# Optimization experiments

Hardware: AMD Instinct MI355X
Metric: run time of the kernel (lower is better)

## Reference

```python
import jax, jax.numpy as jnp
import numpy as np

B, N, F = 4096, 128, 3
EPS = 1e-5


def _bn(x, g, b):
    # BatchNorm1d(element_num) on [B, N, C]: channels are dim 1 (the N elements);
    # training-mode stats over dims (0, 2), biased variance (torch default).
    m = x.mean(axis=(0, 2), keepdims=True)
    v = ((x - m) ** 2).mean(axis=(0, 2), keepdims=True)
    return (x - m) / jnp.sqrt(v + EPS) * g[None, :, None] + b[None, :, None]


def _rel(x, W, bvec, psi, phi, wr):
    # f'_i = wr/N * sum_{j != i} (psi*phi * <x_i, x_j>) * relu(unary(x_j))
    n = x.shape[1]
    U = jax.nn.relu(jnp.einsum('bnd,ed->bne', x, W) + bvec)       # [B,N,D]
    S = (psi * phi) * jnp.einsum('bnd,bmd->bnm', x, x)            # [B,N,N]
    S = S * (1.0 - jnp.eye(n, dtype=x.dtype))                     # exclude j == i
    return wr * jnp.einsum('bnm,bmd->bnd', S, U) / n


def setup_inputs() -> dict:
    key = jax.random.key(0)
    ks = iter(jax.random.split(key, 64))
    d1, d2 = 2 * F, 4 * F  # 6, 12

    def w(shape, s=0.1):
        return (jax.random.normal(next(ks), shape, dtype=jnp.float32) * s)

    def scalar():
        return jax.random.uniform(next(ks), (), dtype=jnp.float32)

    inp = {
        'x': jax.random.normal(next(ks), (B, N, F), dtype=jnp.float32),
        'fc1_w': w((d1, F)), 'fc1_b': w((d1,)),
        'bn1_g': jnp.ones((N,), jnp.float32), 'bn1_b': jnp.zeros((N,), jnp.float32),
        'fc2_w': w((d2, d1)), 'fc2_b': w((d2,)),
        'bn2_g': jnp.ones((N,), jnp.float32), 'bn2_b': jnp.zeros((N,), jnp.float32),
        'fc3_w': w((d2, d2)), 'fc3_b': w((d2,)),
        'u1_w': w((d2, d2)), 'u1_b': w((d2,)), 'ps1': scalar(), 'ph1': scalar(), 'wr1': scalar(),
        'u2_w': w((d2, d2)), 'u2_b': w((d2,)), 'ps2': scalar(), 'ph2': scalar(), 'wr2': scalar(),
        'u3_w': w((d2, d2)), 'u3_b': w((d2,)), 'ps3': scalar(), 'ph3': scalar(), 'wr3': scalar(),
        'u4_w': w((d2, d2)), 'u4_b': w((d2,)), 'ps4': scalar(), 'ph4': scalar(), 'wr4': scalar(),
        'fc4_w': w((d1, d2)), 'fc4_b': w((d1,)),
        'bn4_g': jnp.ones((N,), jnp.float32), 'bn4_b': jnp.zeros((N,), jnp.float32),
        'fc5_w': w((F, d1)), 'fc5_b': w((F,)),
        'fc6_w': w((1, F)), 'fc6_b': w((1,)),
        'fc7_w': w((F - 1, F)), 'fc7_b': w((F - 1,)),
        'fc8_w': w((1, F)), 'fc8_b': w((1,)),
    }
    return inp


def reference(x, fc1_w, fc1_b, bn1_g, bn1_b, fc2_w, fc2_b, bn2_g, bn2_b,
              fc3_w, fc3_b,
              u1_w, u1_b, ps1, ph1, wr1,
              u2_w, u2_b, ps2, ph2, wr2,
              u3_w, u3_b, ps3, ph3, wr3,
              u4_w, u4_b, ps4, ph4, wr4,
              fc4_w, fc4_b, bn4_g, bn4_b,
              fc5_w, fc5_b, fc6_w, fc6_b, fc7_w, fc7_b, fc8_w, fc8_b):
    h = jax.nn.relu(_bn(jnp.einsum('bnf,ef->bne', x, fc1_w) + fc1_b, bn1_g, bn1_b))
    h = jax.nn.relu(_bn(jnp.einsum('bnf,ef->bne', h, fc2_w) + fc2_b, bn2_g, bn2_b))
    h = jax.nn.sigmoid(jnp.einsum('bnf,ef->bne', h, fc3_w) + fc3_b)
    h = _rel(h, u1_w, u1_b, ps1, ph1, wr1)
    h = _rel(h, u2_w, u2_b, ps2, ph2, wr2)
    h = _rel(h, u3_w, u3_b, ps3, ph3, wr3)
    h = _rel(h, u4_w, u4_b, ps4, ph4, wr4)
    h = jax.nn.relu(_bn(jnp.einsum('bnf,ef->bne', h, fc4_w) + fc4_b, bn4_g, bn4_b))
    h = jax.nn.relu(jnp.einsum('bnf,ef->bne', h, fc5_w) + fc5_b)
    cls = jnp.einsum('bnf,ef->bne', h, fc6_w) + fc6_b          # [B,N,1]
    geo = jnp.einsum('bnf,ef->bne', h, fc7_w) + fc7_b          # [B,N,F-1]
    res = jnp.concatenate([cls, geo], axis=2)                   # [B,N,F]
    pres = res.max(axis=1)                                      # MaxPool1d over all N -> [B,F]
    pred = jax.nn.sigmoid(pres @ fc8_w.T + fc8_b)               # [B,1]
    return pred
```

## Files before the change

kernel.cpp:

```cpp
#include <hip/hip_runtime.h>
#include <hip/hip_fp16.h>

#define BB 4096
#define NN 128
#define EPS 1e-5f

#define S1 0
#define S2 2048
#define S4 4096
#define A4_OFF 6144

static __device__ __forceinline__ float sigmoidf_(float z){
  return 1.f/(1.f+__expf(-z));
}
static __device__ __forceinline__ float2 h2f2_(unsigned u){
  __half2 h = *reinterpret_cast<__half2*>(&u);
  return __half22float2(h);
}

static __device__ __forceinline__ float fdot2_(unsigned a, unsigned b, float c){
#if defined(__has_builtin)
#if __has_builtin(__builtin_amdgcn_fdot2)
  typedef _Float16 h2v __attribute__((ext_vector_type(2)));
  h2v av = *reinterpret_cast<h2v*>(&a);
  h2v bv = *reinterpret_cast<h2v*>(&b);
  return __builtin_amdgcn_fdot2(av, bv, c, false);
#else
  float2 af = h2f2_(a), bf = h2f2_(b);
  return fmaf(af.y, bf.y, fmaf(af.x, bf.x, c));
#endif
#else
  float2 af = h2f2_(a), bf = h2f2_(b);
  return fmaf(af.y, bf.y, fmaf(af.x, bf.x, c));
#endif
}

__global__ __launch_bounds__(256) void k1(const float* __restrict__ x, const float* __restrict__ w1,
                   const float* __restrict__ b1, float* __restrict__ st){
  __shared__ float bl[512];
  const int t = threadIdx.x;
  const int tid = blockIdx.x*256 + t;
  float W[18], Bv[6];
  #pragma unroll
  for (int i=0;i<18;i++) W[i]=w1[i];
  #pragma unroll
  for (int i=0;i<6;i++) Bv[i]=b1[i];
  float s=0.f, sq=0.f;
  #pragma unroll
  for (int kk=0;kk<2;kk++){
    const int r = tid + kk*262144;
    const float* xr = x + (size_t)r*3;
    float x0=xr[0], x1=xr[1], x2=xr[2];
    #pragma unroll
    for (int e=0;e<6;e++){
      float a = fmaf(x0,W[e*3+0], fmaf(x1,W[e*3+1], fmaf(x2,W[e*3+2], Bv[e])));
      s+=a; sq=fmaf(a,a,sq);
    }
  }
  bl[t]=s; bl[256+t]=sq;
  __syncthreads();
  const int shadow = (blockIdx.x & 7)*256;
  if (t<128) atomicAdd(&st[S1+shadow+t], bl[t]+bl[t+128]);
  else       atomicAdd(&st[S1+shadow+t], bl[t+128]+bl[t+256]);
}

__global__ __launch_bounds__(256) void k2(const float* __restrict__ x,
                   const float* __restrict__ w1, const float* __restrict__ b1,
                   const float* __restrict__ g1, const float* __restrict__ bb1,
                   const float* __restrict__ w2, const float* __restrict__ b2,
                   float* __restrict__ st){
  __shared__ float bl[512];
  const int t = threadIdx.x;
  const int tid = blockIdx.x*256 + t;
  const int n = t & 127;
  float ss=0.f, qs=0.f;
  #pragma unroll
  for (int c=0;c<8;c++){ ss+=st[S1+c*256+n]; qs+=st[S1+c*256+128+n]; }
  const float mean = ss*(1.f/(BB*6));
  const float var  = qs*(1.f/(BB*6)) - mean*mean;
  const float sc = g1[n]*rsqrtf(var+EPS), sh = bb1[n]-mean*sc;
  float W1[18], B1v[6], W2[72], B2v[12];
  #pragma unroll
  for (int i=0;i<18;i++) W1[i]=w1[i];
  #pragma unroll
  for (int i=0;i<6;i++) B1v[i]=b1[i];
  #pragma unroll
  for (int i=0;i<72;i++) W2[i]=w2[i];
  #pragma unroll
  for (int i=0;i<12;i++) B2v[i]=b2[i];
  float s=0.f, sq=0.f;
  #pragma unroll
  for (int kk=0;kk<2;kk++){
    const int r = tid + kk*262144;
    const float* xr = x + (size_t)r*3;
    float x0=xr[0], x1=xr[1], x2=xr[2];
    float h[6];
    #pragma unroll
    for (int e=0;e<6;e++){
      float a = fmaf(x0,W1[e*3+0], fmaf(x1,W1[e*3+1], fmaf(x2,W1[e*3+2], B1v[e])));
      h[e]=fmaxf(fmaf(a,sc,sh),0.f);
    }
    #pragma unroll
    for (int d=0;d<12;d++){
      float z=B2v[d];
      #pragma unroll
      for (int e=0;e<6;e++) z=fmaf(h[e],W2[d*6+e],z);
      s+=z; sq=fmaf(z,z,sq);
    }
  }
  bl[t]=s; bl[256+t]=sq;
  __syncthreads();
  const int shadow = (blockIdx.x & 7)*256;
  if (t<128) atomicAdd(&st[S2+shadow+t], bl[t]+bl[t+128]);
  else       atomicAdd(&st[S2+shadow+t], bl[t+128]+bl[t+256]);
}

__global__ __launch_bounds__(256) void k3(
  const float* __restrict__ x,
  const float* __restrict__ w1, const float* __restrict__ b1,
  const float* __restrict__ g1, const float* __restrict__ bb1,
  const float* __restrict__ w2, const float* __restrict__ b2,
  const float* __restrict__ g2, const float* __restrict__ bb2,
  const float* __restrict__ w3, const float* __restrict__ b3,
  const float* __restrict__ u1w, const float* __restrict__ u1b,
  const float* __restrict__ ps1, const float* __restrict__ ph1, const float* __restrict__ wr1,
  const float* __restrict__ u2w, const float* __restrict__ u2b,
  const float* __restrict__ ps2, const float* __restrict__ ph2, const float* __restrict__ wr2,
  const float* __restrict__ u3w, const float* __restrict__ u3b,
  const float* __restrict__ ps3, const float* __restrict__ ph3, const float* __restrict__ wr3,
  const float* __restrict__ u4w, const float* __restrict__ u4b,
  const float* __restrict__ ps4, const float* __restrict__ ph4, const float* __restrict__ wr4,
  const float* __restrict__ w4, const float* __restrict__ b4,
  __half* __restrict__ a4, float* __restrict__ st)
{
  __shared__ float lds[4][1536];
  const int wave = threadIdx.x >> 6;
  const int lane = threadIdx.x & 63;
  const int b = blockIdx.x*4 + wave;
  unsigned* Xp = (unsigned*)&lds[wave][0];
  unsigned* Up = (unsigned*)&lds[wave][768];
  const int r0 = lane*2, r1 = r0+1;

  float s1a=0,q1a=0,s1b=0,q1b=0,s2a=0,q2a=0,s2b=0,q2b=0;
  #pragma unroll
  for (int c=0;c<8;c++){
    s1a+=st[S1+c*256+r0]; q1a+=st[S1+c*256+128+r0];
    s1b+=st[S1+c*256+r1]; q1b+=st[S1+c*256+128+r1];
    s2a+=st[S2+c*256+r0]; q2a+=st[S2+c*256+128+r0];
    s2b+=st[S2+c*256+r1]; q2b+=st[S2+c*256+128+r1];
  }
  const float inv1 = 1.f/(BB*6), inv2 = 1.f/(BB*12);
  float m = s1a*inv1, v = q1a*inv1 - m*m;
  const float sA0 = g1[r0]*rsqrtf(v+EPS), hA0 = bb1[r0]-m*sA0;
  m = s1b*inv1; v = q1b*inv1 - m*m;
  const float sA1 = g1[r1]*rsqrtf(v+EPS), hA1 = bb1[r1]-m*sA1;
  m = s2a*inv2; v = q2a*inv2 - m*m;
  const float sB0 = g2[r0]*rsqrtf(v+EPS), hB0 = bb2[r0]-m*sB0;
  m = s2b*inv2; v = q2b*inv2 - m*m;
  const float sB1 = g2[r1]*rsqrtf(v+EPS), hB1 = bb2[r1]-m*sB1;

  const float2* xr = (const float2*)(x + ((size_t)b*128 + r0)*3);
  float2 c0=xr[0], c1=xr[1], c2=xr[2];
  const float xa0=c0.x, xa1=c0.y, xa2=c1.x;
  const float xb0=c1.y, xb1=c2.x, xb2=c2.y;

  float X0[12], X1[12];
  {
    float g6a[6], g6b[6];
    #pragma unroll
    for (int e=0;e<6;e++){
      float a0 = fmaf(xa0,w1[e*3+0], fmaf(xa1,w1[e*3+1], fmaf(xa2,w1[e*3+2], b1[e])));
      float a1v= fmaf(xb0,w1[e*3+0], fmaf(xb1,w1[e*3+1], fmaf(xb2,w1[e*3+2], b1[e])));
      g6a[e]=fmaxf(fmaf(a0,sA0,hA0),0.f);
      g6b[e]=fmaxf(fmaf(a1v,sA1,hA1),0.f);
    }
    float h0[12], h1[12];
    #pragma unroll
    for (int d=0;d<12;d++){
      float z0=b2[d], z1=b2[d];
      #pragma unroll
      for (int e=0;e<6;e++){ z0=fmaf(g6a[e],w2[d*6+e],z0); z1=fmaf(g6b[e],w2[d*6+e],z1); }
      h0[d]=fmaxf(fmaf(z0,sB0,hB0),0.f);
      h1[d]=fmaxf(fmaf(z1,sB1,hB1),0.f);
    }
    #pragma unroll
    for (int d=0; d<12; d++){
      float z0=b3[d], z1=b3[d];
      #pragma unroll
      for (int e=0;e<12;e++){ z0=fmaf(h0[e],w3[d*12+e],z0); z1=fmaf(h1[e],w3[d*12+e],z1); }
      X0[d]=sigmoidf_(z0); X1[d]=sigmoidf_(z1);
    }
  }

  const float* UW[4]  = {u1w,u2w,u3w,u4w};
  const float* UBv[4] = {u1b,u2b,u3b,u4b};
  const float cf[4] = {
    wr1[0]*ps1[0]*ph1[0]*(1.f/128.f),
    wr2[0]*ps2[0]*ph2[0]*(1.f/128.f),
    wr3[0]*ps3[0]*ph3[0]*(1.f/128.f),
    wr4[0]*ps4[0]*ph4[0]*(1.f/128.f)
  };

  const int g = lane>>4;
  int kc = lane & 15; if (kc>11) kc=11;

  #pragma unroll
  for (int l=0;l<4;l++){
    const float* uw = UW[l];
    const float* ub = UBv[l];
    const float coef = cf[l];
    float Y0[12], Y1[12];
    {
      float U0[12], U1[12];
      #pragma unroll
      for (int d=0;d<12;d++){
        float z0=ub[d], z1=ub[d];
        #pragma unroll
        for (int e=0;e<12;e++){ z0=fmaf(X0[e],uw[d*12+e],z0); z1=fmaf(X1[e],uw[d*12+e],z1); }
        U0[d]=fmaxf(z0,0.f); U1[d]=fmaxf(z1,0.f);
      }
      float q0=0.f, q1=0.f;
      #pragma unroll
      for (int e=0;e<12;e++){ q0=fmaf(X0[e],X0[e],q0); q1=fmaf(X1[e],X1[e],q1); }
      __half2 hp[12], up[12];
      #pragma unroll
      for (int e=0;e<12;e++){
        hp[e] = __floats2half2_rn(X0[e],X1[e]);
        up[e] = __floats2half2_rn(U0[e],U1[e]);
      }
      {
        const uint4* hpv = (const uint4*)hp;
        const uint4* upv = (const uint4*)up;
        uint4* xw = (uint4*)(Xp + lane*12);
        uint4* uwp = (uint4*)(Up + lane*12);
        xw[0]=hpv[0]; xw[1]=hpv[1]; xw[2]=hpv[2];
        uwp[0]=upv[0]; uwp[1]=upv[1]; uwp[2]=upv[2];
      }
      const float q0c = coef*q0, q1c = coef*q1;
      #pragma unroll
      for (int d=0;d<12;d++){ Y0[d] = -q0c*U0[d]; Y1[d] = -q1c*U1[d]; }
    }

    float mp[12];
    #pragma unroll
    for (int d=0;d<12;d++) mp[d]=0.f;
    #pragma unroll
    for (int i=0;i<16;i++){
      const int p = (g<<4) | ((i+g)&15);
      const unsigned xv2 = Xp[p*12 + kc];
      const uint4* urow = (const uint4*)(Up + p*12);
      uint4 ua=urow[0], ub4=urow[1], uc=urow[2];
      mp[0]=fdot2_(xv2, ua.x, mp[0]);  mp[1]=fdot2_(xv2, ua.y, mp[1]);
      mp[2]=fdot2_(xv2, ua.z, mp[2]);  mp[3]=fdot2_(xv2, ua.w, mp[3]);
      mp[4]=fdot2_(xv2, ub4.x, mp[4]); mp[5]=fdot2_(xv2, ub4.y, mp[5]);
      mp[6]=fdot2_(xv2, ub4.z, mp[6]); mp[7]=fdot2_(xv2, ub4.w, mp[7]);
      mp[8]=fdot2_(xv2, uc.x, mp[8]);  mp[9]=fdot2_(xv2, uc.y, mp[9]);
      mp[10]=fdot2_(xv2, uc.z, mp[10]); mp[11]=fdot2_(xv2, uc.w, mp[11]);
    }
    #pragma unroll
    for (int d=0;d<12;d++) mp[d] += __shfl_xor(mp[d], 16, 64);
    #pragma unroll
    for (int d=0;d<12;d++) mp[d] += __shfl_xor(mp[d], 32, 64);
    #pragma unroll
    for (int d=0;d<12;d++) mp[d] *= coef;

    #pragma unroll
    for (int k=0;k<12;k++){
      const float xa = X0[k], xb = X1[k];
      #pragma unroll
      for (int d=0;d<12;d++){
        const float mv = __int_as_float(__builtin_amdgcn_readlane(__float_as_int(mp[d]), k));
        Y0[d]=fmaf(xa,mv,Y0[d]); Y1[d]=fmaf(xb,mv,Y1[d]);
      }
    }
    #pragma unroll
    for (int d=0;d<12;d++){ X0[d]=Y0[d]; X1[d]=Y1[d]; }
  }

  float z0[6], z1[6];
  float s0=0.f,sq0=0.f,s1=0.f,sq1=0.f;
  #pragma unroll
  for (int e=0;e<6;e++){
    float a0=b4[e], a1v=b4[e];
    #pragma unroll
    for (int d=0;d<12;d++){ a0=fmaf(X0[d],w4[e*12+d],a0); a1v=fmaf(X1[d],w4[e*12+d],a1v); }
    z0[e]=a0; z1[e]=a1v;
    s0+=a0; sq0=fmaf(a0,a0,sq0); s1+=a1v; sq1=fmaf(a1v,a1v,sq1);
  }
  {
    __half2 ha[6];
    ha[0]=__floats2half2_rn(z0[0],z0[1]); ha[1]=__floats2half2_rn(z0[2],z0[3]); ha[2]=__floats2half2_rn(z0[4],z0[5]);
    ha[3]=__floats2half2_rn(z1[0],z1[1]); ha[4]=__floats2half2_rn(z1[2],z1[3]); ha[5]=__floats2half2_rn(z1[4],z1[5]);
    const uint2* hv = (const uint2*)ha;
    uint2* aw = (uint2*)(a4 + ((size_t)b*128 + r0)*6);
    aw[0]=hv[0]; aw[1]=hv[1]; aw[2]=hv[2];
  }

  __syncthreads();
  lds[wave][r0]=s0; lds[wave][r1]=s1;
  lds[wave][128+r0]=sq0; lds[wave][128+r1]=sq1;
  __syncthreads();
  const int t = threadIdx.x;
  const int c = (blockIdx.x & 7)*256;
  atomicAdd(&st[S4 + c + t], lds[0][t]+lds[1][t]+lds[2][t]+lds[3][t]);
}

__global__ __launch_bounds__(256) void k4(
  const __half* __restrict__ a4, const float* __restrict__ g4, const float* __restrict__ bb4,
  const float* __restrict__ w5, const float* __restrict__ b5,
  const float* __restrict__ w6, const float* __restrict__ b6,
  const float* __restrict__ w7, const float* __restrict__ b7,
  const float* __restrict__ w8, const float* __restrict__ b8,
  const float* __restrict__ st, float* __restrict__ out)
{
  const int wave = threadIdx.x>>6, lane = threadIdx.x&63;
  const int b = blockIdx.x*4 + wave;
  const int r0 = lane*2, r1 = r0+1;
  float ss0=0.f, qq0=0.f, ss1=0.f, qq1=0.f;
  #pragma unroll
  for (int cc=0;cc<8;cc++){
    ss0 += st[S4+cc*256+r0];     qq0 += st[S4+cc*256+128+r0];
    ss1 += st[S4+cc*256+r1];     qq1 += st[S4+cc*256+128+r1];
  }
  const float inv = 1.f/(BB*6);
  const float mean0 = ss0*inv, var0 = qq0*inv - mean0*mean0;
  const float sc0 = g4[r0]*rsqrtf(var0+EPS), sh0 = bb4[r0]-mean0*sc0;
  const float mean1 = ss1*inv, var1 = qq1*inv - mean1*mean1;
  const float sc1 = g4[r1]*rsqrtf(var1+EPS), sh1 = bb4[r1]-mean1*sc1;

  const uint2* ar = (const uint2*)(a4 + ((size_t)b*128 + r0)*6);
  uint2 v0=ar[0], v1=ar[1], v2=ar[2];
  float2 f0=h2f2_(v0.x), f1=h2f2_(v0.y), f2=h2f2_(v1.x);
  float2 f3=h2f2_(v1.y), f4=h2f2_(v2.x), f5=h2f2_(v2.y);
  float h0[6] = {f0.x,f0.y,f1.x,f1.y,f2.x,f2.y};
  float h1[6] = {f3.x,f3.y,f4.x,f4.y,f5.x,f5.y};
  #pragma unroll
  for (int e=0;e<6;e++){
    h0[e]=fmaxf(fmaf(h0[e],sc0,sh0),0.f);
    h1[e]=fmaxf(fmaf(h1[e],sc1,sh1),0.f);
  }
  float mx[3];
  {
    float h5a[3], h5b[3];
    #pragma unroll
    for (int f=0;f<3;f++){
      float za=b5[f], zb=b5[f];
      #pragma unroll
      for (int e=0;e<6;e++){ za=fmaf(h0[e],w5[f*6+e],za); zb=fmaf(h1[e],w5[f*6+e],zb); }
      h5a[f]=fmaxf(za,0.f); h5b[f]=fmaxf(zb,0.f);
    }
    float ca=b6[0], cb=b6[0];
    float g0a=b7[0], g0b=b7[0], g1a=b7[1], g1b=b7[1];
    #pragma unroll
    for (int f=0;f<3;f++){
      ca=fmaf(h5a[f],w6[f],ca);   cb=fmaf(h5b[f],w6[f],cb);
      g0a=fmaf(h5a[f],w7[f],g0a); g0b=fmaf(h5b[f],w7[f],g0b);
      g1a=fmaf(h5a[f],w7[3+f],g1a); g1b=fmaf(h5b[f],w7[3+f],g1b);
    }
    mx[0]=fmaxf(ca,cb); mx[1]=fmaxf(g0a,g0b); mx[2]=fmaxf(g1a,g1b);
  }
  #pragma unroll
  for (int off=32; off>0; off>>=1){
    mx[0]=fmaxf(mx[0], __shfl_xor(mx[0],off,64));
    mx[1]=fmaxf(mx[1], __shfl_xor(mx[1],off,64));
    mx[2]=fmaxf(mx[2], __shfl_xor(mx[2],off,64));
  }
  if (lane==0){
    float z = b8[0] + mx[0]*w8[0] + mx[1]*w8[1] + mx[2]*w8[2];
    out[b]=sigmoidf_(z);
  }
}

extern "C" void kernel_launch(void* const* d_in, const int* in_sizes, int n_in,
                              void* d_out, int out_size, void* d_ws, size_t ws_size,
                              hipStream_t stream){
  const float* x   = (const float*)d_in[0];
  const float* f1w = (const float*)d_in[1];
  const float* f1b = (const float*)d_in[2];
  const float* g1  = (const float*)d_in[3];
  const float* bb1 = (const float*)d_in[4];
  const float* f2w = (const float*)d_in[5];
  const float* f2b = (const float*)d_in[6];
  const float* g2  = (const float*)d_in[7];
  const float* bb2 = (const float*)d_in[8];
  const float* f3w = (const float*)d_in[9];
  const float* f3b = (const float*)d_in[10];
  const float* u1w = (const float*)d_in[11];
  const float* u1b = (const float*)d_in[12];
  const float* ps1 = (const float*)d_in[13];
  const float* ph1 = (const float*)d_in[14];
  const float* wr1 = (const float*)d_in[15];
  const float* u2w = (const float*)d_in[16];
  const float* u2b = (const float*)d_in[17];
  const float* ps2 = (const float*)d_in[18];
  const float* ph2 = (const float*)d_in[19];
  const float* wr2 = (const float*)d_in[20];
  const float* u3w = (const float*)d_in[21];
  const float* u3b = (const float*)d_in[22];
  const float* ps3 = (const float*)d_in[23];
  const float* ph3 = (const float*)d_in[24];
  const float* wr3 = (const float*)d_in[25];
  const float* u4w = (const float*)d_in[26];
  const float* u4b = (const float*)d_in[27];
  const float* ps4 = (const float*)d_in[28];
  const float* ph4 = (const float*)d_in[29];
  const float* wr4 = (const float*)d_in[30];
  const float* f4w = (const float*)d_in[31];
  const float* f4b = (const float*)d_in[32];
  const float* g4  = (const float*)d_in[33];
  const float* bb4 = (const float*)d_in[34];
  const float* f5w = (const float*)d_in[35];
  const float* f5b = (const float*)d_in[36];
  const float* f6w = (const float*)d_in[37];
  const float* f6b = (const float*)d_in[38];
  const float* f7w = (const float*)d_in[39];
  const float* f7b = (const float*)d_in[40];
  const float* f8w = (const float*)d_in[41];
  const float* f8b = (const float*)d_in[42];

  float* wsf = (float*)d_ws;
  float* st  = wsf;
  __half* a4 = (__half*)(wsf + A4_OFF);
  float* out = (float*)d_out;

  k1<<<dim3(1024), dim3(256), 0, stream>>>(x, f1w, f1b, st);
  k2<<<dim3(1024), dim3(256), 0, stream>>>(x, f1w, f1b, g1, bb1, f2w, f2b, st);
  k3<<<dim3(1024), dim3(256), 0, stream>>>(x, f1w, f1b, g1, bb1, f2w, f2b, g2, bb2,
      f3w, f3b,
      u1w,u1b,ps1,ph1,wr1, u2w,u2b,ps2,ph2,wr2,
      u3w,u3b,ps3,ph3,wr3, u4w,u4b,ps4,ph4,wr4,
      f4w, f4b, a4, st);
  k4<<<dim3(1024), dim3(256), 0, stream>>>(a4, g4, bb4, f5w, f5b,
      f6w, f6b, f7w, f7b, f8w, f8b, st, out);
}
```

Baseline: 199.9 us.

## Fuse four kernels into one cooperative kernel with grid-wide syncs

Replaces the four-kernel pipeline with a single cooperative kernel. Each wave holds one batch's activations in registers across all phases, and grid.sync() separates the BatchNorm statistic reductions. This avoids recomputing the early layers in later kernels, the fp16 intermediate round-trip through global memory, and three kernel launches. The trade-off is grid-sync cost, plus a requirement that all 1024 blocks be co-resident (256 CUs x 4). If the cooperative launch fails, it falls back to the old kernels.

```diff
diff --git a/kernel.cpp b/kernel.cpp
--- a/kernel.cpp
+++ b/kernel.cpp
@@ -1,5 +1,8 @@
 #include <hip/hip_runtime.h>
 #include <hip/hip_fp16.h>
+#include <hip/hip_cooperative_groups.h>
+
+namespace cg = cooperative_groups;
 
 #define BB 4096
 #define NN 128
@@ -34,6 +37,286 @@
   return fmaf(af.y, bf.y, fmaf(af.x, bf.x, c));
 #endif
 }
+
+__global__ __launch_bounds__(256, 4) void kf(
+  const float* __restrict__ x,
+  const float* __restrict__ w1, const float* __restrict__ b1,
+  const float* __restrict__ g1, const float* __restrict__ bb1,
+  const float* __restrict__ w2, const float* __restrict__ b2,
+  const float* __restrict__ g2, const float* __restrict__ bb2,
+  const float* __restrict__ w3, const float* __restrict__ b3,
+  const float* __restrict__ u1w, const float* __restrict__ u1b,
+  const float* __restrict__ ps1, const float* __restrict__ ph1, const float* __restrict__ wr1,
+  const float* __restrict__ u2w, const float* __restrict__ u2b,
+  const float* __restrict__ ps2, const float* __restrict__ ph2, const float* __restrict__ wr2,
+  const float* __restrict__ u3w, const float* __restrict__ u3b,
+  const float* __restrict__ ps3, const float* __restrict__ ph3, const float* __restrict__ wr3,
+  const float* __restrict__ u4w, const float* __restrict__ u4b,
+  const float* __restrict__ ps4, const float* __restrict__ ph4, const float* __restrict__ wr4,
+  const float* __restrict__ w4, const float* __restrict__ b4,
+  const float* __restrict__ g4, const float* __restrict__ bb4,
+  const float* __restrict__ w5, const float* __restrict__ b5,
+  const float* __restrict__ w6, const float* __restrict__ b6,
+  const float* __restrict__ w7, const float* __restrict__ b7,
+  const float* __restrict__ w8, const float* __restrict__ b8,
+  float* __restrict__ st, float* __restrict__ out)
+{
+  cg::grid_group grid = cg::this_grid();
+  __shared__ float lds[4][1536];
+  const int t = threadIdx.x;
+  const int wave = t >> 6, lane = t & 63;
+  const int b = blockIdx.x*4 + wave;
+  const int r0 = lane*2, r1 = r0+1;
+  const int shadow = (blockIdx.x & 7)*256;
+  unsigned* Xp = (unsigned*)&lds[wave][0];
+  unsigned* Up = (unsigned*)&lds[wave][768];
+
+  const float2* xr = (const float2*)(x + ((size_t)b*128 + r0)*3);
+  float2 c0=xr[0], c1=xr[1], c2=xr[2];
+  const float xa0=c0.x, xa1=c0.y, xa2=c1.x;
+  const float xb0=c1.y, xb1=c2.x, xb2=c2.y;
+
+  float a6a[6], a6b[6];
+  {
+    float s0=0.f,q0=0.f,s1v=0.f,q1=0.f;
+    #pragma unroll
+    for (int e=0;e<6;e++){
+      float va = fmaf(xa0,w1[e*3+0], fmaf(xa1,w1[e*3+1], fmaf(xa2,w1[e*3+2], b1[e])));
+      float vb = fmaf(xb0,w1[e*3+0], fmaf(xb1,w1[e*3+1], fmaf(xb2,w1[e*3+2], b1[e])));
+      a6a[e]=va; a6b[e]=vb;
+      s0+=va; q0=fmaf(va,va,q0);
+      s1v+=vb; q1=fmaf(vb,vb,q1);
+    }
+    lds[wave][r0]=s0; lds[wave][r1]=s1v;
+    lds[wave][128+r0]=q0; lds[wave][128+r1]=q1;
+    __syncthreads();
+    atomicAdd(&st[S1 + shadow + t], lds[0][t]+lds[1][t]+lds[2][t]+lds[3][t]);
+  }
+  grid.sync();
+
+  float z0[12], z1[12];
+  {
+    float sa=0.f,qa=0.f,sb=0.f,qb=0.f;
+    #pragma unroll
+    for (int c=0;c<8;c++){
+      sa+=st[S1+c*256+r0]; qa+=st[S1+c*256+128+r0];
+      sb+=st[S1+c*256+r1]; qb+=st[S1+c*256+128+r1];
+    }
+    const float inv1 = 1.f/(BB*6);
+    float m=sa*inv1, v=qa*inv1-m*m;
+    const float sA0=g1[r0]*rsqrtf(v+EPS), hA0=bb1[r0]-m*sA0;
+    m=sb*inv1; v=qb*inv1-m*m;
+    const float sA1=g1[r1]*rsqrtf(v+EPS), hA1=bb1[r1]-m*sA1;
+
+    float h0[6], h1[6];
+    #pragma unroll
+    for (int e=0;e<6;e++){
+      h0[e]=fmaxf(fmaf(a6a[e],sA0,hA0),0.f);
+      h1[e]=fmaxf(fmaf(a6b[e],sA1,hA1),0.f);
+    }
+    float s0=0.f,q0=0.f,s1v=0.f,q1=0.f;
+    #pragma unroll
+    for (int d=0;d<12;d++){
+      float za=b2[d], zb=b2[d];
+      #pragma unroll
+      for (int e=0;e<6;e++){ za=fmaf(h0[e],w2[d*6+e],za); zb=fmaf(h1[e],w2[d*6+e],zb); }
+      z0[d]=za; z1[d]=zb;
+      s0+=za; q0=fmaf(za,za,q0);
+      s1v+=zb; q1=fmaf(zb,zb,q1);
+    }
+    lds[wave][r0]=s0; lds[wave][r1]=s1v;
+    lds[wave][128+r0]=q0; lds[wave][128+r1]=q1;
+    __syncthreads();
+    atomicAdd(&st[S2 + shadow + t], lds[0][t]+lds[1][t]+lds[2][t]+lds[3][t]);
+  }
+  grid.sync();
+
+  float X0[12], X1[12];
+  {
+    float sa=0.f,qa=0.f,sb=0.f,qb=0.f;
+    #pragma unroll
+    for (int c=0;c<8;c++){
+      sa+=st[S2+c*256+r0]; qa+=st[S2+c*256+128+r0];
+      sb+=st[S2+c*256+r1]; qb+=st[S2+c*256+128+r1];
+    }
+    const float inv2 = 1.f/(BB*12);
+    float m=sa*inv2, v=qa*inv2-m*m;
+    const float sB0=g2[r0]*rsqrtf(v+EPS), hB0=bb2[r0]-m*sB0;
+    m=sb*inv2; v=qb*inv2-m*m;
+    const float sB1=g2[r1]*rsqrtf(v+EPS), hB1=bb2[r1]-m*sB1;
+
+    float h0[12], h1[12];
+    #pragma unroll
+    for (int d=0;d<12;d++){
+      h0[d]=fmaxf(fmaf(z0[d],sB0,hB0),0.f);
+      h1[d]=fmaxf(fmaf(z1[d],sB1,hB1),0.f);
+    }
+    #pragma unroll
+    for (int d=0;d<12;d++){
+      float za=b3[d], zb=b3[d];
+      #pragma unroll
+      for (int e=0;e<12;e++){ za=fmaf(h0[e],w3[d*12+e],za); zb=fmaf(h1[e],w3[d*12+e],zb); }
+      X0[d]=sigmoidf_(za); X1[d]=sigmoidf_(zb);
+    }
+  }
+
+  const float* UW[4]  = {u1w,u2w,u3w,u4w};
+  const float* UBv[4] = {u1b,u2b,u3b,u4b};
+  const float cf[4] = {
+    wr1[0]*ps1[0]*ph1[0]*(1.f/128.f),
+    wr2[0]*ps2[0]*ph2[0]*(1.f/128.f),
+    wr3[0]*ps3[0]*ph3[0]*(1.f/128.f),
+    wr4[0]*ps4[0]*ph4[0]*(1.f/128.f)
+  };
+
+  const int g = lane>>4;
+  int kc = lane & 15; if (kc>11) kc=11;
+
+  #pragma unroll
+  for (int l=0;l<4;l++){
+    const float* uw = UW[l];
+    const float* ub = UBv[l];
+    const float coef = cf[l];
+    float Y0[12], Y1[12];
+    {
+      float U0[12], U1[12];
+      #pragma unroll
+      for (int d=0;d<12;d++){
+        float za=ub[d], zb=ub[d];
+        #pragma unroll
+        for (int e=0;e<12;e++){ za=fmaf(X0[e],uw[d*12+e],za); zb=fmaf(X1[e],uw[d*12+e],zb); }
+        U0[d]=fmaxf(za,0.f); U1[d]=fmaxf(zb,0.f);
+      }
+      float q0=0.f, q1=0.f;
+      #pragma unroll
+      for (int e=0;e<12;e++){ q0=fmaf(X0[e],X0[e],q0); q1=fmaf(X1[e],X1[e],q1); }
+      __half2 hp[12], up[12];
+      #pragma unroll
+      for (int e=0;e<12;e++){
+        hp[e] = __floats2half2_rn(X0[e],X1[e]);
+        up[e] = __floats2half2_rn(U0[e],U1[e]);
+      }
+      {
+        const uint4* hpv = (const uint4*)hp;
+        const uint4* upv = (const uint4*)up;
+        uint4* xw  = (uint4*)(Xp + lane*12);
+        uint4* uwp = (uint4*)(Up + lane*12);
+        xw[0]=hpv[0]; xw[1]=hpv[1]; xw[2]=hpv[2];
+        uwp[0]=upv[0]; uwp[1]=upv[1]; uwp[2]=upv[2];
+      }
+      const float q0c = coef*q0, q1c = coef*q1;
+      #pragma unroll
+      for (int d=0;d<12;d++){ Y0[d] = -q0c*U0[d]; Y1[d] = -q1c*U1[d]; }
+    }
+
+    float mp[12];
+    #pragma unroll
+    for (int d=0;d<12;d++) mp[d]=0.f;
+    #pragma unroll
+    for (int i=0;i<16;i++){
+      const int p = (g<<4) | ((i+g)&15);
+      const unsigned xv2 = Xp[p*12 + kc];
+      const uint4* urow = (const uint4*)(Up + p*12);
+      uint4 ua=urow[0], ub4=urow[1], uc=urow[2];
+      mp[0]=fdot2_(xv2, ua.x, mp[0]);  mp[1]=fdot2_(xv2, ua.y, mp[1]);
+      mp[2]=fdot2_(xv2, ua.z, mp[2]);  mp[3]=fdot2_(xv2, ua.w, mp[3]);
+      mp[4]=fdot2_(xv2, ub4.x, mp[4]); mp[5]=fdot2_(xv2, ub4.y, mp[5]);
+      mp[6]=fdot2_(xv2, ub4.z, mp[6]); mp[7]=fdot2_(xv2, ub4.w, mp[7]);
+      mp[8]=fdot2_(xv2, uc.x, mp[8]);  mp[9]=fdot2_(xv2, uc.y, mp[9]);
+      mp[10]=fdot2_(xv2, uc.z, mp[10]); mp[11]=fdot2_(xv2, uc.w, mp[11]);
+    }
+    #pragma unroll
+    for (int d=0;d<12;d++) mp[d] += __shfl_xor(mp[d], 16, 64);
+    #pragma unroll
+    for (int d=0;d<12;d++) mp[d] += __shfl_xor(mp[d], 32, 64);
+    #pragma unroll
+    for (int d=0;d<12;d++) mp[d] *= coef;
+
+    #pragma unroll
+    for (int k=0;k<12;k++){
+      const float xa = X0[k], xb = X1[k];
+      #pragma unroll
+      for (int d=0;d<12;d++){
+        const float mv = __int_as_float(__builtin_amdgcn_readlane(__float_as_int(mp[d]), k));
+        Y0[d]=fmaf(xa,mv,Y0[d]); Y1[d]=fmaf(xb,mv,Y1[d]);
+      }
+    }
+    #pragma unroll
+    for (int d=0;d<12;d++){ X0[d]=Y0[d]; X1[d]=Y1[d]; }
+  }
+
+  float z4a[6], z4b[6];
+  {
+    float s0=0.f,q0=0.f,s1v=0.f,q1=0.f;
+    #pragma unroll
+    for (int e=0;e<6;e++){
+      float a0=b4[e], a1v=b4[e];
+      #pragma unroll
+      for (int d=0;d<12;d++){ a0=fmaf(X0[d],w4[e*12+d],a0); a1v=fmaf(X1[d],w4[e*12+d],a1v); }
+      z4a[e]=a0; z4b[e]=a1v;
+      s0+=a0; q0=fmaf(a0,a0,q0);
+      s1v+=a1v; q1=fmaf(a1v,a1v,q1);
+    }
+    __syncthreads();
+    lds[wave][r0]=s0; lds[wave][r1]=s1v;
+    lds[wave][128+r0]=q0; lds[wave][128+r1]=q1;
+    __syncthreads();
+    atomicAdd(&st[S4 + shadow + t], lds[0][t]+lds[1][t]+lds[2][t]+lds[3][t]);
+  }
+  grid.sync();
+
+  {
+    float ss0=0.f,qq0=0.f,ss1=0.f,qq1=0.f;
+    #pragma unroll
+    for (int cc=0;cc<8;cc++){
+      ss0+=st[S4+cc*256+r0]; qq0+=st[S4+cc*256+128+r0];
+      ss1+=st[S4+cc*256+r1]; qq1+=st[S4+cc*256+128+r1];
+    }
+    const float inv = 1.f/(BB*6);
+    const float mean0=ss0*inv, var0=qq0*inv-mean0*mean0;
+    const float sc0=g4[r0]*rsqrtf(var0+EPS), sh0=bb4[r0]-mean0*sc0;
+    const float mean1=ss1*inv, var1=qq1*inv-mean1*mean1;
+    const float sc1=g4[r1]*rsqrtf(var1+EPS), sh1=bb4[r1]-mean1*sc1;
+
+    float h0[6], h1[6];
+    #pragma unroll
+    for (int e=0;e<6;e++){
+      h0[e]=fmaxf(fmaf(z4a[e],sc0,sh0),0.f);
+      h1[e]=fmaxf(fmaf(z4b[e],sc1,sh1),0.f);
+    }
+    float mx[3];
+    {
+      float h5a[3], h5b[3];
+      #pragma unroll
+      for (int f=0;f<3;f++){
+        float za=b5[f], zb=b5[f];
+        #pragma unroll
+        for (int e=0;e<6;e++){ za=fmaf(h0[e],w5[f*6+e],za); zb=fmaf(h1[e],w5[f*6+e],zb); }
+        h5a[f]=fmaxf(za,0.f); h5b[f]=fmaxf(zb,0.f);
+      }
+      float ca=b6[0], cb=b6[0];
+      float g0a=b7[0], g0b=b7[0], g1a=b7[1], g1b=b7[1];
+      #pragma unroll
+      for (int f=0;f<3;f++){
+        ca=fmaf(h5a[f],w6[f],ca);   cb=fmaf(h5b[f],w6[f],cb);
+        g0a=fmaf(h5a[f],w7[f],g0a); g0b=fmaf(h5b[f],w7[f],g0b);
+        g1a=fmaf(h5a[f],w7[3+f],g1a); g1b=fmaf(h5b[f],w7[3+f],g1b);
+      }
+      mx[0]=fmaxf(ca,cb); mx[1]=fmaxf(g0a,g0b); mx[2]=fmaxf(g1a,g1b);
+    }
+    #pragma unroll
+    for (int off=32; off>0; off>>=1){
+      mx[0]=fmaxf(mx[0], __shfl_xor(mx[0],off,64));
+      mx[1]=fmaxf(mx[1], __shfl_xor(mx[1],off,64));
+      mx[2]=fmaxf(mx[2], __shfl_xor(mx[2],off,64));
+    }
+    if (lane==0){
+      float z = b8[0] + mx[0]*w8[0] + mx[1]*w8[1] + mx[2]*w8[2];
+      out[b]=sigmoidf_(z);
+    }
+  }
+}
+
 
 __global__ __launch_bounds__(256) void k1(const float* __restrict__ x, const float* __restrict__ w1,
                    const float* __restrict__ b1, float* __restrict__ st){
@@ -423,13 +706,38 @@
   __half* a4 = (__half*)(wsf + A4_OFF);
   float* out = (float*)d_out;
 
-  k1<<<dim3(1024), dim3(256), 0, stream>>>(x, f1w, f1b, st);
-  k2<<<dim3(1024), dim3(256), 0, stream>>>(x, f1w, f1b, g1, bb1, f2w, f2b, st);
-  k3<<<dim3(1024), dim3(256), 0, stream>>>(x, f1w, f1b, g1, bb1, f2w, f2b, g2, bb2,
-      f3w, f3b,
-      u1w,u1b,ps1,ph1,wr1, u2w,u2b,ps2,ph2,wr2,
-      u3w,u3b,ps3,ph3,wr3, u4w,u4b,ps4,ph4,wr4,
-      f4w, f4b, a4, st);
-  k4<<<dim3(1024), dim3(256), 0, stream>>>(a4, g4, bb4, f5w, f5b,
-      f6w, f6b, f7w, f7b, f8w, f8b, st, out);
-}
+  static int coop_ok = 1;
+  if (coop_ok){
+    void* args[] = {
+      (void*)&x,
+      (void*)&f1w, (void*)&f1b, (void*)&g1,  (void*)&bb1,
+      (void*)&f2w, (void*)&f2b, (void*)&g2,  (void*)&bb2,
+      (void*)&f3w, (void*)&f3b,
+      (void*)&u1w, (void*)&u1b, (void*)&ps1, (void*)&ph1, (void*)&wr1,
+      (void*)&u2w, (void*)&u2b, (void*)&ps2, (void*)&ph2, (void*)&wr2,
+      (void*)&u3w, (void*)&u3b, (void*)&ps3, (void*)&ph3, (void*)&wr3,
+      (void*)&u4w, (void*)&u4b, (void*)&ps4, (void*)&ph4, (void*)&wr4,
+      (void*)&f4w, (void*)&f4b, (void*)&g4,  (void*)&bb4,
+      (void*)&f5w, (void*)&f5b, (void*)&f6w, (void*)&f6b,
+      (void*)&f7w, (void*)&f7b, (void*)&f8w, (void*)&f8b,
+      (void*)&st, (void*)&out
+    };
+    hipError_t e = hipLaunchCooperativeKernel((const void*)kf, dim3(1024), dim3(256),
+                                              args, 0, stream);
+    if (e != hipSuccess){
+      coop_ok = 0;
+      (void)hipGetLastError();
+    }
+  }
+  if (!coop_ok){
+    k1<<<dim3(1024), dim3(256), 0, stream>>>(x, f1w, f1b, st);
+    k2<<<dim3(1024), dim3(256), 0, stream>>>(x, f1w, f1b, g1, bb1, f2w, f2b, st);
+    k3<<<dim3(1024), dim3(256), 0, stream>>>(x, f1w, f1b, g1, bb1, f2w, f2b, g2, bb2,
+        f3w, f3b,
+        u1w,u1b,ps1,ph1,wr1, u2w,u2b,ps2,ph2,wr2,
+        u3w,u3b,ps3,ph3,wr3, u4w,u4b,ps4,ph4,wr4,
+        f4w, f4b, a4, st);
+    k4<<<dim3(1024), dim3(256), 0, stream>>>(a4, g4, bb4, f5w, f5b,
+        f6w, f6b, f7w, f7b, f8w, f8b, st, out);
+  }
+}
```

Result: no change. 197.7 us (-1.1%).
